# Performance work log

Measured on AMD Instinct MI355X. Metric: run time of the kernel, lower is better.

The kernel has to match this reference:

```python
import jax, jax.numpy as jnp
import numpy as np

# dims: N atoms, LDIM=(lmax+1)^2=16 spherical index, C channels,
# E atom types, LOUT output irrep index (16), K* = CG parameter counts
N, LDIM, C = 2048, 16, 64
E, LOUT = 4, 16
K3, K2, K1 = 23, 5, 2


def _sparse(key, shape, density):
    # random sparse CG-like coupling tensor (stand-in for e3nn U_matrix_real)
    kv, km = jax.random.split(key)
    v = jax.random.normal(kv, shape, dtype=jnp.float32)
    m = (jax.random.uniform(km, shape) < density).astype(jnp.float32)
    return v * m


def setup_inputs() -> dict:
    key = jax.random.key(0)
    ks = jax.random.split(key, 8)
    x = jax.random.normal(ks[0], (N, LDIM, C), dtype=jnp.float32)
    atom_types = jax.random.randint(ks[1], (N,), 0, E)
    U3 = _sparse(ks[2], (LOUT, LDIM, LDIM, LDIM, K3), 0.05)
    U2 = _sparse(ks[3], (LOUT, LDIM, LDIM, K2), 0.10)
    U1 = _sparse(ks[4], (LOUT, LDIM, K1), 0.20)
    W3 = jax.random.normal(ks[5], (E, K3, C), dtype=jnp.float32) / np.float32(np.sqrt(K3))
    W2 = jax.random.normal(ks[6], (E, K2, C), dtype=jnp.float32) / np.float32(np.sqrt(K2))
    W1 = jax.random.normal(ks[7], (E, K1, C), dtype=jnp.float32) / np.float32(np.sqrt(K1))
    return {"x": x, "atom_types": atom_types, "U3": U3, "U2": U2, "U1": U1,
            "W3": W3, "W2": W2, "W1": W1}


def reference(x, atom_types, U3, U2, U1, W3, W2, W1):
    # MACE correlation-3 symmetric contraction with per-atom-type weights:
    # out[n,c,L] = sum_{ijkw} U3[L,i,j,k,w] W3[t_n,w,c] x_i x_j x_k
    #            + sum_{ijw}  U2[L,i,j,w]   W2[t_n,w,c] x_i x_j
    #            + sum_{iw}   U1[L,i,w]     W1[t_n,w,c] x_i
    xc = jnp.swapaxes(x, 1, 2)                      # [N, C, 16]
    xx = jnp.einsum('nci,ncj->ncij', xc, xc)        # [N, C, 16, 16]

    # order-2 term (per-atom weight gather = irregular access)
    w2n = W2[atom_types]                            # [N, K2, C]
    t2 = jnp.einsum('Lijw,ncij->ncLw', U2, xx)      # [N, C, LOUT, K2]
    out = jnp.einsum('ncLw,nwc->ncL', t2, w2n)

    # order-1 term
    w1n = W1[atom_types]                            # [N, K1, C]
    t1 = jnp.einsum('Liw,nci->ncLw', U1, xc)        # [N, C, LOUT, K1]
    out = out + jnp.einsum('ncLw,nwc->ncL', t1, w1n)

    # order-3 term: pre-contract CG tensor with per-element weights, then
    # loop over the small fixed set of atom types (masked accumulate)
    A3 = jnp.einsum('Lijkw,ewc->ecLijk', U3, W3)    # [E, C, LOUT, 16,16,16]
    for e in range(W3.shape[0]):
        mask = (atom_types == e).astype(x.dtype)[:, None, None]  # [N,1,1]
        t3 = jnp.einsum('cLijk,ncij->ncLk', A3[e], xx)           # [N,C,LOUT,16]
        out = out + mask * jnp.einsum('ncLk,nck->ncL', t3, xc)
    return jnp.swapaxes(out, 1, 2)                  # [N, LOUT, C]
```

## Files before the change

kernel.cpp:

```cpp
#include <hip/hip_runtime.h>
#include <hip/hip_fp16.h>

#define NATOMS 2048
#define CCH    64
#define NE     4

#define NP    136
#define K3DIM 2176
#define M2B   2176
#define M1B   2312
#define KTOT  2328
#define KPAD  2336
#define NSTEP 73
#define MAXBS 12

typedef _Float16 f16x8 __attribute__((ext_vector_type(8)));
typedef float f32x4 __attribute__((ext_vector_type(4)));

__host__ __device__ constexpr int pair_i(int p){ int i=0, rem=p; while (rem >= 16-i){ rem -= 16-i; ++i; } return i; }
__host__ __device__ constexpr int pair_j(int p){ int i=0, rem=p; while (rem >= 16-i){ rem -= 16-i; ++i; } return i+rem; }

struct PTab { unsigned v[68]; };
__host__ __device__ constexpr PTab make_ptab(){
  PTab t{};
  for (int s = 0; s < 68; ++s){
    int p0 = 2*s, p1 = 2*s + 1;
    t.v[s] = (unsigned)(pair_i(p0) | (pair_j(p0)<<5) | (pair_i(p1)<<10) | (pair_j(p1)<<15));
  }
  return t;
}
__device__ __constant__ PTab ptab = make_ptab();

__device__ __forceinline__ __half2 uh(unsigned u){ union{unsigned x;__half2 h;}c; c.x=u; return c.h; }

__device__ __forceinline__ void slot_decode(const int* counts, int g,
                                            int& e, int& b0, int& cnt, int& ns){
  int c0 = counts[0], c1 = counts[1], c2 = counts[2], c3 = counts[3];
  int n0 = (c0+255)>>8, n1 = (c1+255)>>8, n2 = (c2+255)>>8, n3 = (c3+255)>>8;
  ns = n0 + n1 + n2 + n3;
  if (g < n0){ e = 0; b0 = g*256; cnt = c0; }
  else if (g < n0+n1){ e = 1; b0 = (g-n0)*256; cnt = c1; }
  else if (g < n0+n1+n2){ e = 2; b0 = (g-n0-n1)*256; cnt = c2; }
  else { e = 3; b0 = (g-n0-n1-n2)*256; cnt = c3; }
}

__device__ __forceinline__ void pack2(unsigned a, unsigned b, unsigned& lo, unsigned& hi){
  lo = (a & 0xFFFFu) | (b << 16);
  hi = (a >> 16) | (b & 0xFFFF0000u);
}

__global__ __launch_bounds__(256) void prep_all(
    const int* __restrict__ types, int* __restrict__ counts, int* __restrict__ bins,
    const float* __restrict__ U3, const float* __restrict__ U2, const float* __restrict__ U1,
    const float* __restrict__ W3, const float* __restrict__ W2, const float* __restrict__ W1,
    unsigned int* __restrict__ Bbuf, const float* __restrict__ x, unsigned* __restrict__ xTu){
  __shared__ char smem[33280];
  int blk = blockIdx.x;
  int tid = threadIdx.x;

  if (blk == 0){
    int (*hist)[4] = (int(*)[4])smem;
    int ty[8];
    int h0=0,h1=0,h2=0,h3=0;
#pragma unroll
    for (int q = 0; q < 8; ++q){
      int t = types[tid*8 + q] & 3;
      ty[q] = t;
      h0 += (t==0); h1 += (t==1); h2 += (t==2); h3 += (t==3);
    }
    hist[tid][0]=h0; hist[tid][1]=h1; hist[tid][2]=h2; hist[tid][3]=h3;
    __syncthreads();
    if (tid == 0){
      int r0=0,r1=0,r2=0,r3=0;
      for (int t = 0; t < 256; ++t){
        int a=hist[t][0], b=hist[t][1], c2=hist[t][2], d=hist[t][3];
        hist[t][0]=r0; hist[t][1]=r1; hist[t][2]=r2; hist[t][3]=r3;
        r0+=a; r1+=b; r2+=c2; r3+=d;
      }
      counts[0]=r0; counts[1]=r1; counts[2]=r2; counts[3]=r3;
    }
    __syncthreads();
    int p0=hist[tid][0], p1=hist[tid][1], p2=hist[tid][2], p3=hist[tid][3];
#pragma unroll
    for (int q = 0; q < 8; ++q){
      int n = tid*8 + q, t = ty[q];
      int pos;
      if      (t==0) pos = p0++;
      else if (t==1) pos = p1++;
      else if (t==2) pos = p2++;
      else           pos = p3++;
      bins[t*NATOMS + pos] = n;
    }
    return;
  }

  if (blk <= NSTEP*NE){
    int fid = blk - 1;
    int s = fid % NSTEP, e = fid / NSTEP;
    int l = tid >> 2, r = tid & 3, g = l >> 4, L = l & 15;
    int m0 = 32*s + 8*g + 2*r;
    float (*WL)[CCH] = (float(*)[CCH])smem;

    for (int t = tid; t < 33*CCH; t += 256){
      int row = t >> 6, cc = t & 63;
      float v = 0.f;
      if (row < 23)      v = W3[((size_t)e*23 + row)*CCH + cc];
      else if (row < 28) v = W2[((size_t)e*5 + (row-23))*CCH + cc];
      else if (row < 30) v = W1[((size_t)e*2 + (row-28))*CCH + cc];
      WL[row][cc] = v;
    }
    __syncthreads();

    float u0[24], u1[24];
#pragma unroll
    for (int w = 0; w < 24; ++w){ u0[w] = 0.f; u1[w] = 0.f; }

    if (s < 68){
      int p = m0 >> 4, k = m0 & 15;
      int i = 0, rem = p; while (rem >= 16 - i){ rem -= 16 - i; ++i; }
      int j = i + rem;
      const float* rA = &U3[((((size_t)L*16 + i)*16 + j)*16 + k)*23];
      if (i < j){
        const float* rB = &U3[((((size_t)L*16 + j)*16 + i)*16 + k)*23];
#pragma unroll
        for (int w = 0; w < 23; ++w){
          u0[w] = rA[w]      + rB[w];
          u1[w] = rA[23 + w] + rB[23 + w];
        }
      } else {
#pragma unroll
        for (int w = 0; w < 23; ++w){
          u0[w] = rA[w];
          u1[w] = rA[23 + w];
        }
      }
    } else {
      if (m0 < M1B){
        int p2a = m0 - M2B;
        int i = 0, rem = p2a; while (rem >= 16 - i){ rem -= 16 - i; ++i; }
        int j = i + rem;
#pragma unroll
        for (int w = 0; w < 5; ++w){
          float vv = U2[(((size_t)L*16 + i)*16 + j)*5 + w];
          if (i < j) vv += U2[(((size_t)L*16 + j)*16 + i)*5 + w];
          u0[w] = vv;
        }
        int p2b = p2a + 1;
        i = 0; rem = p2b; while (rem >= 16 - i){ rem -= 16 - i; ++i; }
        j = i + rem;
#pragma unroll
        for (int w = 0; w < 5; ++w){
          float vv = U2[(((size_t)L*16 + i)*16 + j)*5 + w];
          if (i < j) vv += U2[(((size_t)L*16 + j)*16 + i)*5 + w];
          u1[w] = vv;
        }
      } else if (m0 < KTOT){
        int i = m0 - M1B;
        u0[0] = U1[((size_t)L*16 + i)*2 + 0];
        u0[1] = U1[((size_t)L*16 + i)*2 + 1];
        u1[0] = U1[((size_t)L*16 + i + 1)*2 + 0];
        u1[1] = U1[((size_t)L*16 + i + 1)*2 + 1];
      }
    }

    const size_t ostride = (size_t)NSTEP*64*4;
    size_t obase = (((size_t)(e*CCH)*NSTEP + s)*64 + l)*4 + r;

    if (s < 68){
      for (int cc0 = 0; cc0 < CCH; cc0 += 4){
        float a0[4] = {0,0,0,0}, a1[4] = {0,0,0,0};
#pragma unroll
        for (int w = 0; w < 23; ++w){
#pragma unroll
          for (int q = 0; q < 4; ++q){
            float wv = WL[w][cc0+q];
            a0[q] += u0[w]*wv; a1[q] += u1[w]*wv;
          }
        }
#pragma unroll
        for (int q = 0; q < 4; ++q){
          union { __half2 h; unsigned int u; } hu;
          hu.h = __halves2half2(__float2half(a0[q]), __float2half(a1[q]));
          Bbuf[obase + (size_t)(cc0+q)*ostride] = hu.u;
        }
      }
    } else {
      int wbase = (m0 < M1B) ? 23 : 28;
      for (int cc0 = 0; cc0 < CCH; cc0 += 4){
        float a0[4] = {0,0,0,0}, a1[4] = {0,0,0,0};
#pragma unroll
        for (int w = 0; w < 5; ++w){
#pragma unroll
          for (int q = 0; q < 4; ++q){
            float wv = WL[wbase + w][cc0+q];
            a0[q] += u0[w]*wv; a1[q] += u1[w]*wv;
          }
        }
#pragma unroll
        for (int q = 0; q < 4; ++q){
          union { __half2 h; unsigned int u; } hu;
          hu.h = __halves2half2(__float2half(a0[q]), __float2half(a1[q]));
          Bbuf[obase + (size_t)(cc0+q)*ostride] = hu.u;
        }
      }
    }
    return;
  }

  int xb = blk - 1 - NSTEP*NE;
  int n0 = xb * 16;

  __half (*ls)[1040] = (__half(*)[1040])smem;
  int a_loc = tid >> 4, i = tid & 15;
  int n = n0 + a_loc;
  {
    const float4* src = (const float4*)(x + (size_t)n*1024 + (size_t)i*64);
#pragma unroll
    for (int q = 0; q < 16; ++q){
      float4 v = src[q];
      int c = q*4;
      ls[a_loc][(c+0)*16 + i] = __float2half(v.x);
      ls[a_loc][(c+1)*16 + i] = __float2half(v.y);
      ls[a_loc][(c+2)*16 + i] = __float2half(v.z);
      ls[a_loc][(c+3)*16 + i] = __float2half(v.w);
    }
  }
  __syncthreads();

  int wid = tid >> 6, lane = tid & 63;
  for (int cp = 0; cp < 16; ++cp){
    int c = cp*4 + wid;
#pragma unroll
    for (int h = 0; h < 2; ++h){
      int a = h*8 + (lane >> 3), i2 = lane & 7;
      __half lo = ls[a][c*16 + 2*i2];
      __half hi = ls[a][c*16 + 2*i2 + 1];
      union { __half2 h2; unsigned u; } pk;
      pk.h2 = __halves2half2(lo, hi);
      xTu[((size_t)c*NATOMS + n0 + a)*8 + i2] = pk.u;
    }
  }
}

__global__ __launch_bounds__(256, 4) void main9_kernel(
    const unsigned* __restrict__ xTu, const int* __restrict__ counts,
    const int* __restrict__ bins, const uint4* __restrict__ Bbuf,
    float* __restrict__ out){
  int v = (blockIdx.x & 7) * 96 + (blockIdx.x >> 3);
  int c = v / MAXBS;
  int g = v % MAXBS;
  int e, b0, cnt, ns;
  slot_decode(counts, g, e, b0, cnt, ns);
  if (g >= ns) return;

  int tid = threadIdx.x;
  int wid = tid >> 6, lane = tid & 63;

  __shared__ uint2 xe[256][19];
  __shared__ unsigned ltab[160];

  bool hi_half = (lane & 16) != 0;
  bool gsel    = (lane & 32) != 0;

  const uint4* xbase = (const uint4*)xTu;
  uint4 tv0[4], tv1[4];
  __half2 xsel[4][4];
#pragma unroll
  for (int T = 0; T < 4; ++T){
    int row = b0 + wid*64 + T*16 + (lane & 15);
    int n = (row < cnt) ? bins[e*NATOMS + row] : -1;
    if (n >= 0){
      const uint4* xr = xbase + ((size_t)c*NATOMS + n)*2;
      tv0[T] = xr[0];
      tv1[T] = xr[1];
    } else {
      tv0[T] = make_uint4(0,0,0,0);
      tv1[T] = make_uint4(0,0,0,0);
    }
    xsel[T][0] = uh(hi_half ? tv1[T].x : tv0[T].x);
    xsel[T][1] = uh(hi_half ? tv1[T].y : tv0[T].y);
    xsel[T][2] = uh(hi_half ? tv1[T].z : tv0[T].z);
    xsel[T][3] = uh(hi_half ? tv1[T].w : tv0[T].w);
  }
  {
    unsigned alo, ahi, blo, bhi;
    pack2(tv0[0].x, tv0[1].x, alo, ahi); pack2(tv0[2].x, tv0[3].x, blo, bhi);
    xe[tid][0] = make_uint2(alo, blo); xe[tid][1] = make_uint2(ahi, bhi);
    pack2(tv0[0].y, tv0[1].y, alo, ahi); pack2(tv0[2].y, tv0[3].y, blo, bhi);
    xe[tid][2] = make_uint2(alo, blo); xe[tid][3] = make_uint2(ahi, bhi);
    pack2(tv0[0].z, tv0[1].z, alo, ahi); pack2(tv0[2].z, tv0[3].z, blo, bhi);
    xe[tid][4] = make_uint2(alo, blo); xe[tid][5] = make_uint2(ahi, bhi);
    pack2(tv0[0].w, tv0[1].w, alo, ahi); pack2(tv0[2].w, tv0[3].w, blo, bhi);
    xe[tid][6] = make_uint2(alo, blo); xe[tid][7] = make_uint2(ahi, bhi);
    pack2(tv1[0].x, tv1[1].x, alo, ahi); pack2(tv1[2].x, tv1[3].x, blo, bhi);
    xe[tid][8] = make_uint2(alo, blo); xe[tid][9] = make_uint2(ahi, bhi);
    pack2(tv1[0].y, tv1[1].y, alo, ahi); pack2(tv1[2].y, tv1[3].y, blo, bhi);
    xe[tid][10] = make_uint2(alo, blo); xe[tid][11] = make_uint2(ahi, bhi);
    pack2(tv1[0].z, tv1[1].z, alo, ahi); pack2(tv1[2].z, tv1[3].z, blo, bhi);
    xe[tid][12] = make_uint2(alo, blo); xe[tid][13] = make_uint2(ahi, bhi);
    pack2(tv1[0].w, tv1[1].w, alo, ahi); pack2(tv1[2].w, tv1[3].w, blo, bhi);
    xe[tid][14] = make_uint2(alo, blo); xe[tid][15] = make_uint2(ahi, bhi);
    xe[tid][16] = make_uint2(0x3C003C00u, 0x3C003C00u);
    xe[tid][17] = make_uint2(0u, 0u);
  }
  if (tid < 160){
    unsigned ij;
    if (tid < NP)        ij = (unsigned)(pair_i(tid) | (pair_j(tid) << 8));
    else if (tid < 152)  ij = (unsigned)((tid - NP) | (16 << 8));
    else                 ij = (unsigned)(17 | (17 << 8));
    ltab[tid] = ij;
  }
  __syncthreads();

  const uint4* Bpan = Bbuf + (size_t)(e*CCH + c)*NSTEP*64 + lane;

  f32x4 acc0 = {0,0,0,0}, acc1 = {0,0,0,0}, acc2 = {0,0,0,0}, acc3 = {0,0,0,0};

  uint4 pb0 = Bpan[0*64], pb1 = Bpan[1*64], pb2 = Bpan[2*64], pb3 = Bpan[3*64];

  unsigned pk0 = ptab.v[0];
  int is = gsel ? ((pk0>>10)&31) : (pk0&31);
  int js = gsel ? ((pk0>>15)&31) : ((pk0>>5)&31);
  uint2 pi = xe[tid][is], pj = xe[tid][js];

#pragma unroll 4
  for (int s = 0; s < 68; ++s){
    uint2 npi = pi, npj = pj;
    if (s < 67){
      unsigned pk = ptab.v[s+1];
      int is2 = gsel ? ((pk>>10)&31) : (pk&31);
      int js2 = gsel ? ((pk>>15)&31) : ((pk>>5)&31);
      npi = xe[tid][is2]; npj = xe[tid][js2];
    }
    uint4 cur = pb0; pb0 = pb1; pb1 = pb2; pb2 = pb3;
    int ld = (s + 4 <= 72) ? (s + 4) : 72;
    pb3 = Bpan[(size_t)ld*64];

    __half2 p01 = __hmul2(uh(pi.x), uh(pj.x));
    __half2 p23 = __hmul2(uh(pi.y), uh(pj.y));

    union { uint4 u; f16x8 h; } bc; bc.u = cur;
    __half2 pv0 = __half2half2(__low2half(p01));
    __half2 pv1 = __half2half2(__high2half(p01));
    __half2 pv2 = __half2half2(__low2half(p23));
    __half2 pv3 = __half2half2(__high2half(p23));
    union { __half2 h[4]; f16x8 v; } u0, u1, u2, u3;
#pragma unroll
    for (int q = 0; q < 4; ++q){
      u0.h[q] = __hmul2(pv0, xsel[0][q]);
      u1.h[q] = __hmul2(pv1, xsel[1][q]);
      u2.h[q] = __hmul2(pv2, xsel[2][q]);
      u3.h[q] = __hmul2(pv3, xsel[3][q]);
    }
    acc0 = __builtin_amdgcn_mfma_f32_16x16x32_f16(u0.v, bc.h, acc0, 0,0,0);
    acc1 = __builtin_amdgcn_mfma_f32_16x16x32_f16(u1.v, bc.h, acc1, 0,0,0);
    acc2 = __builtin_amdgcn_mfma_f32_16x16x32_f16(u2.v, bc.h, acc2, 0,0,0);
    acc3 = __builtin_amdgcn_mfma_f32_16x16x32_f16(u3.v, bc.h, acc3, 0,0,0);
    pi = npi; pj = npj;
  }

  int g2 = (lane >> 4) & 3;
#pragma unroll
  for (int s = 68; s < 73; ++s){
    uint4 cur = pb0; pb0 = pb1; pb1 = pb2; pb2 = pb3;
    pb3 = Bpan[(size_t)72*64];
    int mb = 32*s + 8*g2 - M2B;
    union { uint4 u; f16x8 h; } bc; bc.u = cur;
    union { __half2 h[4]; f16x8 v; } u0, u1, u2, u3;
#pragma unroll
    for (int q = 0; q < 4; ++q){
      unsigned ta = ltab[mb + 2*q], tb = ltab[mb + 2*q + 1];
      uint2 A = xe[tid][ta & 255], B = xe[tid][ta >> 8];
      uint2 C = xe[tid][tb & 255], D = xe[tid][tb >> 8];
      __half2 pa01 = __hmul2(uh(A.x), uh(B.x));
      __half2 pb01 = __hmul2(uh(C.x), uh(D.x));
      __half2 pa23 = __hmul2(uh(A.y), uh(B.y));
      __half2 pb23 = __hmul2(uh(C.y), uh(D.y));
      u0.h[q] = __halves2half2(__low2half(pa01),  __low2half(pb01));
      u1.h[q] = __halves2half2(__high2half(pa01), __high2half(pb01));
      u2.h[q] = __halves2half2(__low2half(pa23),  __low2half(pb23));
      u3.h[q] = __halves2half2(__high2half(pa23), __high2half(pb23));
    }
    acc0 = __builtin_amdgcn_mfma_f32_16x16x32_f16(u0.v, bc.h, acc0, 0,0,0);
    acc1 = __builtin_amdgcn_mfma_f32_16x16x32_f16(u1.v, bc.h, acc1, 0,0,0);
    acc2 = __builtin_amdgcn_mfma_f32_16x16x32_f16(u2.v, bc.h, acc2, 0,0,0);
    acc3 = __builtin_amdgcn_mfma_f32_16x16x32_f16(u3.v, bc.h, acc3, 0,0,0);
  }

  int gp = lane >> 4, L = lane & 15;
#pragma unroll
  for (int T = 0; T < 4; ++T){
    f32x4 a = (T==0) ? acc0 : (T==1) ? acc1 : (T==2) ? acc2 : acc3;
    int rb = b0 + wid*64 + T*16;
#pragma unroll
    for (int r = 0; r < 4; ++r){
      int row = rb + 4*gp + r;
      if (row < cnt){
        int n = bins[e*NATOMS + row];
        out[((size_t)n*16 + L)*CCH + c] = a[r];
      }
    }
  }
}

extern "C" void kernel_launch(void* const* d_in, const int* in_sizes, int n_in,
                              void* d_out, int out_size, void* d_ws, size_t ws_size,
                              hipStream_t stream){
  const float* x   = (const float*)d_in[0];
  const int* types = (const int*)d_in[1];
  const float* U3  = (const float*)d_in[2];
  const float* U2  = (const float*)d_in[3];
  const float* U1  = (const float*)d_in[4];
  const float* W3  = (const float*)d_in[5];
  const float* W2  = (const float*)d_in[6];
  const float* W1  = (const float*)d_in[7];
  float* out = (float*)d_out;

  char* ws = (char*)d_ws;
  int* counts  = (int*)ws;
  int* bins    = (int*)(ws + 1024);

  const size_t bbOff   = 33792;
  const size_t bbBytes = (size_t)NE * 64 * NSTEP * 64 * 16;
  const size_t xtOff   = bbOff + bbBytes;

  unsigned int* Bbuf = (unsigned int*)(ws + bbOff);
  unsigned* xTu = (unsigned*)(ws + xtOff);

  prep_all<<<1 + NSTEP*NE + 128, 256, 0, stream>>>(types, counts, bins,
                                                   U3, U2, U1, W3, W2, W1,
                                                   Bbuf, x, xTu);
  main9_kernel<<<MAXBS*64, 256, 0, stream>>>(xTu, counts, bins, (const uint4*)Bbuf, out);
}
```

Before: 62.32 us.

## Fuse prep and main kernels into one cooperative launch with grid sync

Merges the preprocessing kernel (binning, weight folding, x transpose) and the main contraction kernel into a single cooperative kernel separated by a grid-wide barrier, with a two-kernel fallback if cooperative launch fails. The aim is to remove the second launch and the gap between kernels. It also splits each fold block across two channel halves so more blocks share that work. In exchange, every block must stay resident at once, the shared-memory footprint is sized for the largest phase, and the grid sync has its own cost.

```diff
diff --git a/kernel.cpp b/kernel.cpp
--- a/kernel.cpp
+++ b/kernel.cpp
@@ -1,5 +1,8 @@
 #include <hip/hip_runtime.h>
 #include <hip/hip_fp16.h>
+#include <hip/hip_cooperative_groups.h>
+
+namespace cg = cooperative_groups;
 
 #define NATOMS 2048
 #define CCH    64
@@ -13,6 +16,7 @@
 #define KPAD  2336
 #define NSTEP 73
 #define MAXBS 12
+#define GRIDN 768
 
 typedef _Float16 f16x8 __attribute__((ext_vector_type(8)));
 typedef float f32x4 __attribute__((ext_vector_type(4)));
@@ -49,167 +53,161 @@
   hi = (a >> 16) | (b & 0xFFFF0000u);
 }
 
-__global__ __launch_bounds__(256) void prep_all(
-    const int* __restrict__ types, int* __restrict__ counts, int* __restrict__ bins,
+__device__ __forceinline__ void do_bin(const int* __restrict__ types, int* __restrict__ counts,
+                                       int* __restrict__ bins, char* smem, int tid){
+  int (*hist)[4] = (int(*)[4])smem;
+  int ty[8];
+  int h0=0,h1=0,h2=0,h3=0;
+#pragma unroll
+  for (int q = 0; q < 8; ++q){
+    int t = types[tid*8 + q] & 3;
+    ty[q] = t;
+    h0 += (t==0); h1 += (t==1); h2 += (t==2); h3 += (t==3);
+  }
+  hist[tid][0]=h0; hist[tid][1]=h1; hist[tid][2]=h2; hist[tid][3]=h3;
+  __syncthreads();
+  if (tid == 0){
+    int r0=0,r1=0,r2=0,r3=0;
+    for (int t = 0; t < 256; ++t){
+      int a=hist[t][0], b=hist[t][1], c2=hist[t][2], d=hist[t][3];
+      hist[t][0]=r0; hist[t][1]=r1; hist[t][2]=r2; hist[t][3]=r3;
+      r0+=a; r1+=b; r2+=c2; r3+=d;
+    }
+    counts[0]=r0; counts[1]=r1; counts[2]=r2; counts[3]=r3;
+  }
+  __syncthreads();
+  int p0=hist[tid][0], p1=hist[tid][1], p2=hist[tid][2], p3=hist[tid][3];
+#pragma unroll
+  for (int q = 0; q < 8; ++q){
+    int n = tid*8 + q, t = ty[q];
+    int pos;
+    if      (t==0) pos = p0++;
+    else if (t==1) pos = p1++;
+    else if (t==2) pos = p2++;
+    else           pos = p3++;
+    bins[t*NATOMS + pos] = n;
+  }
+}
+
+__device__ __forceinline__ void do_fold(int fid,
     const float* __restrict__ U3, const float* __restrict__ U2, const float* __restrict__ U1,
     const float* __restrict__ W3, const float* __restrict__ W2, const float* __restrict__ W1,
-    unsigned int* __restrict__ Bbuf, const float* __restrict__ x, unsigned* __restrict__ xTu){
-  __shared__ char smem[33280];
-  int blk = blockIdx.x;
-  int tid = threadIdx.x;
-
-  if (blk == 0){
-    int (*hist)[4] = (int(*)[4])smem;
-    int ty[8];
-    int h0=0,h1=0,h2=0,h3=0;
-#pragma unroll
-    for (int q = 0; q < 8; ++q){
-      int t = types[tid*8 + q] & 3;
-      ty[q] = t;
-      h0 += (t==0); h1 += (t==1); h2 += (t==2); h3 += (t==3);
-    }
-    hist[tid][0]=h0; hist[tid][1]=h1; hist[tid][2]=h2; hist[tid][3]=h3;
-    __syncthreads();
-    if (tid == 0){
-      int r0=0,r1=0,r2=0,r3=0;
-      for (int t = 0; t < 256; ++t){
-        int a=hist[t][0], b=hist[t][1], c2=hist[t][2], d=hist[t][3];
-        hist[t][0]=r0; hist[t][1]=r1; hist[t][2]=r2; hist[t][3]=r3;
-        r0+=a; r1+=b; r2+=c2; r3+=d;
-      }
-      counts[0]=r0; counts[1]=r1; counts[2]=r2; counts[3]=r3;
-    }
-    __syncthreads();
-    int p0=hist[tid][0], p1=hist[tid][1], p2=hist[tid][2], p3=hist[tid][3];
-#pragma unroll
-    for (int q = 0; q < 8; ++q){
-      int n = tid*8 + q, t = ty[q];
-      int pos;
-      if      (t==0) pos = p0++;
-      else if (t==1) pos = p1++;
-      else if (t==2) pos = p2++;
-      else           pos = p3++;
-      bins[t*NATOMS + pos] = n;
-    }
-    return;
-  }
-
-  if (blk <= NSTEP*NE){
-    int fid = blk - 1;
-    int s = fid % NSTEP, e = fid / NSTEP;
-    int l = tid >> 2, r = tid & 3, g = l >> 4, L = l & 15;
-    int m0 = 32*s + 8*g + 2*r;
-    float (*WL)[CCH] = (float(*)[CCH])smem;
-
-    for (int t = tid; t < 33*CCH; t += 256){
-      int row = t >> 6, cc = t & 63;
-      float v = 0.f;
-      if (row < 23)      v = W3[((size_t)e*23 + row)*CCH + cc];
-      else if (row < 28) v = W2[((size_t)e*5 + (row-23))*CCH + cc];
-      else if (row < 30) v = W1[((size_t)e*2 + (row-28))*CCH + cc];
-      WL[row][cc] = v;
-    }
-    __syncthreads();
-
-    float u0[24], u1[24];
-#pragma unroll
-    for (int w = 0; w < 24; ++w){ u0[w] = 0.f; u1[w] = 0.f; }
-
-    if (s < 68){
-      int p = m0 >> 4, k = m0 & 15;
-      int i = 0, rem = p; while (rem >= 16 - i){ rem -= 16 - i; ++i; }
+    unsigned int* __restrict__ Bbuf, char* smem, int tid){
+  int se = fid >> 1, half = fid & 1;
+  int s = se % NSTEP, e = se / NSTEP;
+  int ccBase = half * 32;
+  int l = tid >> 2, r = tid & 3, g = l >> 4, L = l & 15;
+  int m0 = 32*s + 8*g + 2*r;
+  float (*WL)[CCH] = (float(*)[CCH])smem;
+
+  for (int t = tid; t < 33*CCH; t += 256){
+    int row = t >> 6, cc = t & 63;
+    float v = 0.f;
+    if (row < 23)      v = W3[((size_t)e*23 + row)*CCH + cc];
+    else if (row < 28) v = W2[((size_t)e*5 + (row-23))*CCH + cc];
+    else if (row < 30) v = W1[((size_t)e*2 + (row-28))*CCH + cc];
+    WL[row][cc] = v;
+  }
+  __syncthreads();
+
+  float u0[24], u1[24];
+#pragma unroll
+  for (int w = 0; w < 24; ++w){ u0[w] = 0.f; u1[w] = 0.f; }
+
+  if (s < 68){
+    int p = m0 >> 4, k = m0 & 15;
+    int i = 0, rem = p; while (rem >= 16 - i){ rem -= 16 - i; ++i; }
+    int j = i + rem;
+    const float* rA = &U3[((((size_t)L*16 + i)*16 + j)*16 + k)*23];
+    if (i < j){
+      const float* rB = &U3[((((size_t)L*16 + j)*16 + i)*16 + k)*23];
+#pragma unroll
+      for (int w = 0; w < 23; ++w){
+        u0[w] = rA[w]      + rB[w];
+        u1[w] = rA[23 + w] + rB[23 + w];
+      }
+    } else {
+#pragma unroll
+      for (int w = 0; w < 23; ++w){
+        u0[w] = rA[w];
+        u1[w] = rA[23 + w];
+      }
+    }
+  } else {
+    if (m0 < M1B){
+      int p2a = m0 - M2B;
+      int i = 0, rem = p2a; while (rem >= 16 - i){ rem -= 16 - i; ++i; }
       int j = i + rem;
-      const float* rA = &U3[((((size_t)L*16 + i)*16 + j)*16 + k)*23];
-      if (i < j){
-        const float* rB = &U3[((((size_t)L*16 + j)*16 + i)*16 + k)*23];
-#pragma unroll
-        for (int w = 0; w < 23; ++w){
-          u0[w] = rA[w]      + rB[w];
-          u1[w] = rA[23 + w] + rB[23 + w];
+#pragma unroll
+      for (int w = 0; w < 5; ++w){
+        float vv = U2[(((size_t)L*16 + i)*16 + j)*5 + w];
+        if (i < j) vv += U2[(((size_t)L*16 + j)*16 + i)*5 + w];
+        u0[w] = vv;
+      }
+      int p2b = p2a + 1;
+      i = 0; rem = p2b; while (rem >= 16 - i){ rem -= 16 - i; ++i; }
+      j = i + rem;
+#pragma unroll
+      for (int w = 0; w < 5; ++w){
+        float vv = U2[(((size_t)L*16 + i)*16 + j)*5 + w];
+        if (i < j) vv += U2[(((size_t)L*16 + j)*16 + i)*5 + w];
+        u1[w] = vv;
+      }
+    } else if (m0 < KTOT){
+      int i = m0 - M1B;
+      u0[0] = U1[((size_t)L*16 + i)*2 + 0];
+      u0[1] = U1[((size_t)L*16 + i)*2 + 1];
+      u1[0] = U1[((size_t)L*16 + i + 1)*2 + 0];
+      u1[1] = U1[((size_t)L*16 + i + 1)*2 + 1];
+    }
+  }
+
+  const size_t ostride = (size_t)NSTEP*64*4;
+  size_t obase = (((size_t)(e*CCH)*NSTEP + s)*64 + l)*4 + r;
+
+  if (s < 68){
+    for (int cc0 = ccBase; cc0 < ccBase + 32; cc0 += 4){
+      float a0[4] = {0,0,0,0}, a1[4] = {0,0,0,0};
+#pragma unroll
+      for (int w = 0; w < 23; ++w){
+#pragma unroll
+        for (int q = 0; q < 4; ++q){
+          float wv = WL[w][cc0+q];
+          a0[q] += u0[w]*wv; a1[q] += u1[w]*wv;
         }
-      } else {
-#pragma unroll
-        for (int w = 0; w < 23; ++w){
-          u0[w] = rA[w];
-          u1[w] = rA[23 + w];
+      }
+#pragma unroll
+      for (int q = 0; q < 4; ++q){
+        union { __half2 h; unsigned int u; } hu;
+        hu.h = __halves2half2(__float2half(a0[q]), __float2half(a1[q]));
+        Bbuf[obase + (size_t)(cc0+q)*ostride] = hu.u;
+      }
+    }
+  } else {
+    int wbase = (m0 < M1B) ? 23 : 28;
+    for (int cc0 = ccBase; cc0 < ccBase + 32; cc0 += 4){
+      float a0[4] = {0,0,0,0}, a1[4] = {0,0,0,0};
+#pragma unroll
+      for (int w = 0; w < 5; ++w){
+#pragma unroll
+        for (int q = 0; q < 4; ++q){
+          float wv = WL[wbase + w][cc0+q];
+          a0[q] += u0[w]*wv; a1[q] += u1[w]*wv;
         }
       }
-    } else {
-      if (m0 < M1B){
-        int p2a = m0 - M2B;
-        int i = 0, rem = p2a; while (rem >= 16 - i){ rem -= 16 - i; ++i; }
-        int j = i + rem;
-#pragma unroll
-        for (int w = 0; w < 5; ++w){
-          float vv = U2[(((size_t)L*16 + i)*16 + j)*5 + w];
-          if (i < j) vv += U2[(((size_t)L*16 + j)*16 + i)*5 + w];
-          u0[w] = vv;
-        }
-        int p2b = p2a + 1;
-        i = 0; rem = p2b; while (rem >= 16 - i){ rem -= 16 - i; ++i; }
-        j = i + rem;
-#pragma unroll
-        for (int w = 0; w < 5; ++w){
-          float vv = U2[(((size_t)L*16 + i)*16 + j)*5 + w];
-          if (i < j) vv += U2[(((size_t)L*16 + j)*16 + i)*5 + w];
-          u1[w] = vv;
-        }
-      } else if (m0 < KTOT){
-        int i = m0 - M1B;
-        u0[0] = U1[((size_t)L*16 + i)*2 + 0];
-        u0[1] = U1[((size_t)L*16 + i)*2 + 1];
-        u1[0] = U1[((size_t)L*16 + i + 1)*2 + 0];
-        u1[1] = U1[((size_t)L*16 + i + 1)*2 + 1];
-      }
-    }
-
-    const size_t ostride = (size_t)NSTEP*64*4;
-    size_t obase = (((size_t)(e*CCH)*NSTEP + s)*64 + l)*4 + r;
-
-    if (s < 68){
-      for (int cc0 = 0; cc0 < CCH; cc0 += 4){
-        float a0[4] = {0,0,0,0}, a1[4] = {0,0,0,0};
-#pragma unroll
-        for (int w = 0; w < 23; ++w){
-#pragma unroll
-          for (int q = 0; q < 4; ++q){
-            float wv = WL[w][cc0+q];
-            a0[q] += u0[w]*wv; a1[q] += u1[w]*wv;
-          }
-        }
-#pragma unroll
-        for (int q = 0; q < 4; ++q){
-          union { __half2 h; unsigned int u; } hu;
-          hu.h = __halves2half2(__float2half(a0[q]), __float2half(a1[q]));
-          Bbuf[obase + (size_t)(cc0+q)*ostride] = hu.u;
-        }
-      }
-    } else {
-      int wbase = (m0 < M1B) ? 23 : 28;
-      for (int cc0 = 0; cc0 < CCH; cc0 += 4){
-        float a0[4] = {0,0,0,0}, a1[4] = {0,0,0,0};
-#pragma unroll
-        for (int w = 0; w < 5; ++w){
-#pragma unroll
-          for (int q = 0; q < 4; ++q){
-            float wv = WL[wbase + w][cc0+q];
-            a0[q] += u0[w]*wv; a1[q] += u1[w]*wv;
-          }
-        }
-#pragma unroll
-        for (int q = 0; q < 4; ++q){
-          union { __half2 h; unsigned int u; } hu;
-          hu.h = __halves2half2(__float2half(a0[q]), __float2half(a1[q]));
-          Bbuf[obase + (size_t)(cc0+q)*ostride] = hu.u;
-        }
-      }
-    }
-    return;
-  }
-
-  int xb = blk - 1 - NSTEP*NE;
+#pragma unroll
+      for (int q = 0; q < 4; ++q){
+        union { __half2 h; unsigned int u; } hu;
+        hu.h = __halves2half2(__float2half(a0[q]), __float2half(a1[q]));
+        Bbuf[obase + (size_t)(cc0+q)*ostride] = hu.u;
+      }
+    }
+  }
+}
+
+__device__ __forceinline__ void do_xpose(int xb, const float* __restrict__ x,
+                                         unsigned* __restrict__ xTu, char* smem, int tid){
   int n0 = xb * 16;
-
   __half (*ls)[1040] = (__half(*)[1040])smem;
   int a_loc = tid >> 4, i = tid & 15;
   int n = n0 + a_loc;
@@ -226,7 +224,6 @@
     }
   }
   __syncthreads();
-
   int wid = tid >> 6, lane = tid & 63;
   for (int cp = 0; cp < 16; ++cp){
     int c = cp*4 + wid;
@@ -242,22 +239,20 @@
   }
 }
 
-__global__ __launch_bounds__(256, 4) void main9_kernel(
+__device__ __forceinline__ void do_main(int blk, int tid,
     const unsigned* __restrict__ xTu, const int* __restrict__ counts,
-    const int* __restrict__ bins, const uint4* __restrict__ Bbuf,
-    float* __restrict__ out){
-  int v = (blockIdx.x & 7) * 96 + (blockIdx.x >> 3);
+    const int* __restrict__ bins, const uint4* __restrict__ Bb,
+    float* __restrict__ out, char* smem){
+  int v = (blk & 7) * 96 + (blk >> 3);
   int c = v / MAXBS;
   int g = v % MAXBS;
   int e, b0, cnt, ns;
   slot_decode(counts, g, e, b0, cnt, ns);
   if (g >= ns) return;
 
-  int tid = threadIdx.x;
   int wid = tid >> 6, lane = tid & 63;
-
-  __shared__ uint2 xe[256][19];
-  __shared__ unsigned ltab[160];
+  uint2 (*xe)[19] = (uint2(*)[19])smem;
+  unsigned* ltab  = (unsigned*)(smem + 38912);
 
   bool hi_half = (lane & 16) != 0;
   bool gsel    = (lane & 32) != 0;
@@ -282,6 +277,7 @@
     xsel[T][2] = uh(hi_half ? tv1[T].z : tv0[T].z);
     xsel[T][3] = uh(hi_half ? tv1[T].w : tv0[T].w);
   }
+  __syncthreads();
   {
     unsigned alo, ahi, blo, bhi;
     pack2(tv0[0].x, tv0[1].x, alo, ahi); pack2(tv0[2].x, tv0[3].x, blo, bhi);
@@ -312,10 +308,9 @@
   }
   __syncthreads();
 
-  const uint4* Bpan = Bbuf + (size_t)(e*CCH + c)*NSTEP*64 + lane;
+  const uint4* Bpan = Bb + (size_t)(e*CCH + c)*NSTEP*64 + lane;
 
   f32x4 acc0 = {0,0,0,0}, acc1 = {0,0,0,0}, acc2 = {0,0,0,0}, acc3 = {0,0,0,0};
-
   uint4 pb0 = Bpan[0*64], pb1 = Bpan[1*64], pb2 = Bpan[2*64], pb3 = Bpan[3*64];
 
   unsigned pk0 = ptab.v[0];
@@ -403,6 +398,46 @@
   }
 }
 
+__global__ __launch_bounds__(256, 4) void fused_kernel(
+    const int* __restrict__ types, int* __restrict__ counts, int* __restrict__ bins,
+    const float* __restrict__ U3, const float* __restrict__ U2, const float* __restrict__ U1,
+    const float* __restrict__ W3, const float* __restrict__ W2, const float* __restrict__ W1,
+    unsigned int* __restrict__ Bbuf, const float* __restrict__ x, unsigned* __restrict__ xTu,
+    float* __restrict__ out){
+  __shared__ char smem[39552];
+  int blk = blockIdx.x;
+  int tid = threadIdx.x;
+
+  if (blk == 0)                       do_bin(types, counts, bins, smem, tid);
+  else if (blk <= 2*NSTEP*NE)         do_fold(blk - 1, U3, U2, U1, W3, W2, W1, Bbuf, smem, tid);
+  else if (blk <= 2*NSTEP*NE + 128)   do_xpose(blk - 1 - 2*NSTEP*NE, x, xTu, smem, tid);
+
+  cg::this_grid().sync();
+
+  do_main(blk, tid, xTu, counts, bins, (const uint4*)Bbuf, out, smem);
+}
+
+__global__ __launch_bounds__(256) void prep_all(
+    const int* __restrict__ types, int* __restrict__ counts, int* __restrict__ bins,
+    const float* __restrict__ U3, const float* __restrict__ U2, const float* __restrict__ U1,
+    const float* __restrict__ W3, const float* __restrict__ W2, const float* __restrict__ W1,
+    unsigned int* __restrict__ Bbuf, const float* __restrict__ x, unsigned* __restrict__ xTu){
+  __shared__ char smem[39552];
+  int blk = blockIdx.x;
+  int tid = threadIdx.x;
+  if (blk == 0)                       do_bin(types, counts, bins, smem, tid);
+  else if (blk <= 2*NSTEP*NE)         do_fold(blk - 1, U3, U2, U1, W3, W2, W1, Bbuf, smem, tid);
+  else                                do_xpose(blk - 1 - 2*NSTEP*NE, x, xTu, smem, tid);
+}
+
+__global__ __launch_bounds__(256, 4) void main9_kernel(
+    const unsigned* __restrict__ xTu, const int* __restrict__ counts,
+    const int* __restrict__ bins, const uint4* __restrict__ Bbuf,
+    float* __restrict__ out){
+  __shared__ char smem[39552];
+  do_main(blockIdx.x, threadIdx.x, xTu, counts, bins, Bbuf, out, smem);
+}
+
 extern "C" void kernel_launch(void* const* d_in, const int* in_sizes, int n_in,
                               void* d_out, int out_size, void* d_ws, size_t ws_size,
                               hipStream_t stream){
@@ -427,8 +462,17 @@
   unsigned int* Bbuf = (unsigned int*)(ws + bbOff);
   unsigned* xTu = (unsigned*)(ws + xtOff);
 
-  prep_all<<<1 + NSTEP*NE + 128, 256, 0, stream>>>(types, counts, bins,
-                                                   U3, U2, U1, W3, W2, W1,
-                                                   Bbuf, x, xTu);
-  main9_kernel<<<MAXBS*64, 256, 0, stream>>>(xTu, counts, bins, (const uint4*)Bbuf, out);
-}
+  void* args[] = { (void*)&types, (void*)&counts, (void*)&bins,
+                   (void*)&U3, (void*)&U2, (void*)&U1,
+                   (void*)&W3, (void*)&W2, (void*)&W1,
+                   (void*)&Bbuf, (void*)&x, (void*)&xTu, (void*)&out };
+  hipError_t err = hipLaunchCooperativeKernel((void*)fused_kernel, dim3(GRIDN), dim3(256),
+                                              args, 0, stream);
+  if (err != hipSuccess){
+    (void)hipGetLastError();
+    prep_all<<<1 + 2*NSTEP*NE + 128, 256, 0, stream>>>(types, counts, bins,
+                                                       U3, U2, U1, W3, W2, W1,
+                                                       Bbuf, x, xTu);
+    main9_kernel<<<GRIDN, 256, 0, stream>>>(xTu, counts, bins, (const uint4*)Bbuf, out);
+  }
+}
```

Result: slower. 178.6 us (+186.5%).
